# Kernel optimization log

Measured on AMD Instinct MI355X. Metric: run time of the kernel, lower is better.

## Reference

```python
import jax, jax.numpy as jnp
import numpy as np

ALPHA = 0.2          # LeakyReLU negative slope
NEG_INF = -9e15      # mask value used by the torch module


def setup_inputs() -> dict:
    key = jax.random.key(0)
    k_x, k_adj, k_w, k_a = jax.random.split(key, 4)
    B, N, D, L = 8, 2048, 128, 3
    x = jax.random.normal(k_x, (B, N, D), dtype=jnp.float32)
    adj = jax.random.randint(k_adj, (B, N, N), 0, 2, dtype=jnp.int32)
    Wg = jax.random.normal(k_w, (L, D, D), dtype=jnp.float32) * 0.08  # ~Linear init scale
    bg = jnp.zeros((L, D), dtype=jnp.float32)
    attn_a = jax.random.normal(k_a, (L, 2 * D), dtype=jnp.float32) * 0.08
    return {"x": x, "adj": adj, "Wg": Wg, "bg": bg, "attn_a": attn_a}


def reference(x, adj, Wg, bg, attn_a):
    # x: [B,N,D], adj: [B,N,N] int, Wg: [L,D,D], bg: [L,D], attn_a: [L,2D]
    D = x.shape[-1]
    L = Wg.shape[0]
    mask = adj > 0
    for i in range(L):  # small fixed layer loop
        h = jax.nn.relu(x @ Wg[i] + bg[i])                       # [B,N,D]
        # a_input[b,i,j] = [h_i, h_j]; dot with a splits into two rank-1 terms,
        # avoiding the N*N*2D intermediate while computing identical math.
        s1 = h @ attn_a[i, :D]                                   # [B,N]
        s2 = h @ attn_a[i, D:]                                   # [B,N]
        e = jax.nn.leaky_relu(s1[:, :, None] + s2[:, None, :], ALPHA)  # [B,N,N]
        e = jnp.where(mask, e, NEG_INF)
        attn = jax.nn.softmax(e, axis=2)                         # masked softmax over neighbors
        # dropout p=0.0 -> identity
        x = x + jnp.einsum('bij,bjd->bid', attn, h)              # residual update
    return x
```

## Files before the change

kernel.cpp:

```cpp
#include <hip/hip_runtime.h>
#include <stdint.h>

typedef __attribute__((ext_vector_type(8))) short short8;
typedef __attribute__((ext_vector_type(4))) float f32x4;
typedef __attribute__((ext_vector_type(16))) float f32x16;
typedef __attribute__((ext_vector_type(4))) unsigned uint4v;

#define LOG2E 1.4426950408889634f

__device__ __forceinline__ unsigned short f2bf(float f) {
    unsigned u = __float_as_uint(f);
    unsigned r = u + 0x7fffu + ((u >> 16) & 1u);
    return (unsigned short)(r >> 16);
}
__device__ __forceinline__ unsigned fenc(float f) {
    unsigned u = __float_as_uint(f);
    return (u & 0x80000000u) ? ~u : (u | 0x80000000u);
}
__device__ __forceinline__ float fdec(unsigned e) {
    unsigned u = (e & 0x80000000u) ? (e & 0x7fffffffu) : ~e;
    return __uint_as_float(u);
}
__device__ __forceinline__ unsigned cvt_pk_bf16(float lo, float hi) {
    unsigned r;
    asm("v_cvt_pk_bf16_f32 %0, %1, %2" : "=v"(r) : "v"(lo), "v"(hi));
    return r;
}

__global__ __launch_bounds__(256) void k_setup(
    const float* __restrict__ xin, const float* __restrict__ Wf,
    const int* __restrict__ adj, float* __restrict__ xq,
    unsigned short* __restrict__ wTb, unsigned* __restrict__ s2mx,
    unsigned long long* __restrict__ packed)
{
    int blk = blockIdx.x, tid = threadIdx.x;
    if (blk < 2048) {
        int w = (blk * 256 + tid) >> 6;
        int lane = tid & 63;
        for (int k = 0; k < 64; k++) {
            int q = w * 64 + k;
            int row = q >> 5, wd = q & 31;
            int v = adj[row * 2048 + wd * 64 + lane];
            unsigned long long m = __ballot(v > 0);
            if (lane == 0) packed[q] = m;
        }
    } else if (blk < 4096) {
        int e0 = ((blk - 2048) * 256 + tid) * 4;
        *(f32x4*)(xq + e0) = *(const f32x4*)(xin + e0);
    } else if (blk < 4288) {
        int c = (blk - 4096) * 256 + tid;
        int l = c >> 14, rem = c & 16383, n = rem >> 7, k = rem & 127;
        wTb[c] = f2bf(Wf[l * 16384 + k * 128 + n]);
    } else if (tid < 24) {
        s2mx[tid] = fenc(-3e38f);
    }
}

__global__ __launch_bounds__(512) void k_h(
    const float* __restrict__ xq, const unsigned short* __restrict__ wTb,
    const float* __restrict__ bF, const float* __restrict__ aF, int layer,
    unsigned short* __restrict__ hP, float* __restrict__ s1g,
    float* __restrict__ s2g, unsigned* __restrict__ s2mx)
{
    __shared__ short xs[64 * 136];
    __shared__ short wsb[128 * 136];
    __shared__ float s12[2][2][64];
    int blk = blockIdx.x, tid = threadIdx.x;
    int b = blk & 7, rg = blk >> 3;
    int row0 = b * 2048 + rg * 64;
    int lane = tid & 63, quad = lane >> 4, l15 = lane & 15;
    int wv = tid >> 6, rw = wv & 3, ch = wv >> 2;

    for (int c = tid; c < 1024; c += 512) {
        int r = c >> 4, kg = c & 15;
        const float* src = &xq[(row0 + r) * 128 + kg * 8];
        f32x4 v0 = *(const f32x4*)src;
        f32x4 v1 = *(const f32x4*)(src + 4);
        short8 o;
        o[0] = (short)f2bf(v0[0]); o[1] = (short)f2bf(v0[1]);
        o[2] = (short)f2bf(v0[2]); o[3] = (short)f2bf(v0[3]);
        o[4] = (short)f2bf(v1[0]); o[5] = (short)f2bf(v1[1]);
        o[6] = (short)f2bf(v1[2]); o[7] = (short)f2bf(v1[3]);
        *(short8*)&xs[r * 136 + kg * 8] = o;
    }
    const unsigned short* wl = wTb + layer * 16384;
    for (int c = tid; c < 2048; c += 512) {
        int n = c >> 4, kg = c & 15;
        *(short8*)&wsb[n * 136 + kg * 8] = *(const short8*)&wl[n * 128 + kg * 8];
    }
    __syncthreads();

    f32x4 acc[4];
#pragma unroll
    for (int t = 0; t < 4; t++) acc[t] = {0.f, 0.f, 0.f, 0.f};
#pragma unroll
    for (int ks = 0; ks < 4; ks++) {
        short8 af = *(const short8*)&xs[(rw * 16 + l15) * 136 + ks * 32 + quad * 8];
#pragma unroll
        for (int t = 0; t < 4; t++) {
            short8 bf = *(const short8*)&wsb[((ch * 4 + t) * 16 + l15) * 136 + ks * 32 + quad * 8];
            acc[t] = __builtin_amdgcn_mfma_f32_16x16x32_bf16(af, bf, acc[t], 0, 0, 0);
        }
    }

    float s1p[4] = {0.f, 0.f, 0.f, 0.f}, s2p[4] = {0.f, 0.f, 0.f, 0.f};
#pragma unroll
    for (int t = 0; t < 4; t++) {
        int colg = (ch * 4 + t) * 16 + l15;
        float bgf = bF[layer * 128 + colg];
        float a1 = aF[layer * 256 + colg] * LOG2E;
        float a2 = aF[layer * 256 + 128 + colg] * LOG2E;
#pragma unroll
        for (int r = 0; r < 4; r++) {
            float v = acc[t][r] + bgf;
            v = v > 0.f ? v : 0.f;
            acc[t][r] = v;
            s1p[r] = fmaf(v, a1, s1p[r]);
            s2p[r] = fmaf(v, a2, s2p[r]);
        }
    }
#pragma unroll
    for (int r = 0; r < 4; r++) {
#pragma unroll
        for (int off = 1; off < 16; off <<= 1) {
            s1p[r] += __shfl_xor(s1p[r], off, 64);
            s2p[r] += __shfl_xor(s2p[r], off, 64);
        }
    }
    if (l15 == 0) {
#pragma unroll
        for (int r = 0; r < 4; r++) {
            int rloc = rw * 16 + quad * 4 + r;
            s12[0][ch][rloc] = s1p[r];
            s12[1][ch][rloc] = s2p[r];
        }
    }
    __syncthreads();

    short* st = (short*)wsb;
#pragma unroll
    for (int t = 0; t < 4; t++)
#pragma unroll
        for (int r = 0; r < 4; r++)
            st[(rw * 16 + quad * 4 + r) * 130 + (ch * 4 + t) * 16 + l15] = (short)f2bf(acc[t][r]);

    if (tid < 64) {
        float s1 = s12[0][0][tid] + s12[0][1][tid];
        float s2 = s12[1][0][tid] + s12[1][1][tid];
        s1g[row0 + tid] = s1;
        s2g[row0 + tid] = s2;
        float mx = s2;
#pragma unroll
        for (int off = 1; off < 64; off <<= 1)
            mx = fmaxf(mx, __shfl_xor(mx, off, 64));
        if (tid == 0) atomicMax(&s2mx[layer * 8 + b], fenc(mx));
    }
    __syncthreads();
    int jt0 = rg * 4;
    for (int c = tid; c < 1024; c += 512) {
        int t = c >> 8, jl2 = (c >> 6) & 3, sl = c & 63;
        int d = t * 32 + (sl & 31);
        int jloc = jl2 * 16 + (sl >> 5) * 8;
        short8 o;
#pragma unroll
        for (int i = 0; i < 8; i++) o[i] = st[(jloc + i) * 130 + d];
        *(short8*)&hP[(((size_t)(b * 4 + t) * 128 + (jt0 + jl2)) * 64 + sl) * 8] = o;
    }
}

#define GAT_STEP(JL, CUR, NXT)                                                  \
  {                                                                             \
    unsigned b8 = (unsigned)(wdv[CUR] >> joff) & 0xffu;                         \
    float pv[8];                                                                \
    _Pragma("unroll")                                                           \
    for (int jj = 0; jj < 4; jj++) {                                            \
      float v0 = s1fold + sA[CUR][jj];                                          \
      float v1 = s1fold + sB[CUR][jj];                                          \
      pv[jj]     = __builtin_amdgcn_exp2f(fmaxf(v0, fmaf(0.2f, v0, c8)));       \
      pv[jj + 4] = __builtin_amdgcn_exp2f(fmaxf(v1, fmaf(0.2f, v1, c8)));       \
    }                                                                           \
    uint4v pk;                                                                  \
    pk[0] = cvt_pk_bf16(pv[0], pv[1]) & lutq[0][b8];                            \
    pk[1] = cvt_pk_bf16(pv[2], pv[3]) & lutq[1][b8];                            \
    pk[2] = cvt_pk_bf16(pv[4], pv[5]) & lutq[2][b8];                            \
    pk[3] = cvt_pk_bf16(pv[6], pv[7]) & lutq[3][b8];                            \
    short8 af = *(short8*)&pk;                                                  \
    *(short8*)&pshare[CUR][w][lane * 8] = af;                                   \
    ps = __builtin_amdgcn_mfma_f32_32x32x16_bf16(af, onesf, ps, 0, 0, 0);       \
    if ((JL) + 1 < 32) {                                                        \
      wdv[NXT] = prow[(JL) + 1];                                                \
      int j0n = ((JL) + 1) * 64 + joff;                                         \
      sA[NXT] = *(const f32x4*)&s2gb[j0n];                                      \
      sB[NXT] = *(const f32x4*)&s2gb[j0n + 4];                                  \
      _Pragma("unroll")                                                         \
      for (int q = 0; q < 4; q++)                                               \
        bfr[NXT][q] = *(const short8*)&hPb[((size_t)(w * 128 + ((JL) + 1) * 4 + q) * 64 + lane) * 8]; \
    }                                                                           \
    __syncthreads();                                                            \
    _Pragma("unroll")                                                           \
    for (int q = 0; q < 4; q++) {                                               \
      short8 pf = *(short8*)&pshare[CUR][q][lane * 8];                          \
      acc = __builtin_amdgcn_mfma_f32_32x32x16_bf16(pf, bfr[CUR][q], acc, 0, 0, 0); \
    }                                                                           \
  }

__global__ __launch_bounds__(256) void k_attn(
    const unsigned long long* __restrict__ packed,
    const unsigned short* __restrict__ hP, const float* __restrict__ s1g,
    const float* __restrict__ s2g, const unsigned* __restrict__ s2mx,
    int layer, float* __restrict__ xq)
{
    __shared__ unsigned lutq[4][256];
    __shared__ short pshare[2][4][512];
    __shared__ float red_p[4][32];
    int blk = blockIdx.x, tid = threadIdx.x;
    int b = blk & 7, rg = blk >> 3;
    int rowg0 = b * 2048 + rg * 32;
    int w = tid >> 6, lane = tid & 63;
    int col = lane & 31, khalf = lane >> 5;

    {
        unsigned e = (unsigned)tid;
#pragma unroll
        for (int q = 0; q < 4; q++)
            lutq[q][e] = (((e >> (2 * q)) & 1u) ? 0xffffu : 0u) |
                         (((e >> (2 * q + 1)) & 1u) ? 0xffff0000u : 0u);
    }

    float s1v = s1g[rowg0 + col];
    float s2m = fdec(s2mx[layer * 8 + b]);
    float tmh = s1v + s2m;
    float mhat = fmaxf(tmh, 0.2f * tmh);
    float s1fold = s1v - mhat;
    float c8 = -0.8f * mhat;

    short8 onesf;
    {
        short v = (col == 0) ? (short)0x3F80 : (short)0;
        onesf[0]=v;onesf[1]=v;onesf[2]=v;onesf[3]=v;onesf[4]=v;onesf[5]=v;onesf[6]=v;onesf[7]=v;
    }

    const float* s2gb = s2g + b * 2048;
    const unsigned short* hPb = hP + (size_t)b * 4 * 128 * 64 * 8;
    const unsigned long long* prow = packed + (size_t)(rowg0 + col) * 32;
    int joff = w * 16 + khalf * 8;

    f32x16 acc, ps;
#pragma unroll
    for (int r = 0; r < 16; r++) { acc[r] = 0.f; ps[r] = 0.f; }

    unsigned long long wdv[2];
    f32x4 sA[2], sB[2];
    short8 bfr[2][4];

    wdv[0] = prow[0];
    sA[0] = *(const f32x4*)&s2gb[joff];
    sB[0] = *(const f32x4*)&s2gb[joff + 4];
#pragma unroll
    for (int q = 0; q < 4; q++)
        bfr[0][q] = *(const short8*)&hPb[((size_t)(w * 128 + q) * 64 + lane) * 8];
    __syncthreads();

#pragma unroll 1
    for (int jl = 0; jl < 32; jl += 2) {
        GAT_STEP(jl, 0, 1)
        GAT_STEP(jl + 1, 1, 0)
    }

#pragma unroll
    for (int reg = 0; reg < 16; reg++) {
        int row = (reg & 3) + 8 * (reg >> 2) + 4 * khalf;
        if (col == 0) red_p[w][row] = ps[reg];
    }
    __syncthreads();
#pragma unroll
    for (int reg = 0; reg < 16; reg++) {
        int row = (reg & 3) + 8 * (reg >> 2) + 4 * khalf;
        float p = red_p[0][row] + red_p[1][row] + red_p[2][row] + red_p[3][row];
        float rl = p > 0.f ? __builtin_amdgcn_rcpf(p) : 0.f;
        xq[(rowg0 + row) * 128 + w * 32 + col] += acc[reg] * rl;
    }
}

extern "C" void kernel_launch(void* const* d_in, const int* in_sizes, int n_in,
                              void* d_out, int out_size, void* d_ws, size_t ws_size,
                              hipStream_t stream) {
    const void* px = d_in[0];
    int ia = 1; long amax = -1;
    for (int i = 1; i < n_in; i++)
        if ((long)in_sizes[i] > amax) { amax = in_sizes[i]; ia = i; }
    int rem[8]; int m = 0;
    for (int i = 1; i < n_in && m < 8; i++) if (i != ia) rem[m++] = i;
    for (int i = 0; i < m; i++)
        for (int j = i + 1; j < m; j++)
            if (in_sizes[rem[j]] > in_sizes[rem[i]]) { int t = rem[i]; rem[i] = rem[j]; rem[j] = t; }
    const int*   padj = (const int*)((n_in > 1) ? d_in[ia] : d_in[0]);
    const float* pW = (const float*)((m > 0) ? d_in[rem[0]] : d_in[0]);
    const float* pa = (const float*)((m > 1) ? d_in[rem[1]] : d_in[0]);
    const float* pb = (const float*)((m > 2) ? d_in[rem[2]] : d_in[0]);

    float* xq = (float*)d_out;
    char* ws = (char*)d_ws;
    unsigned long long* packed = (unsigned long long*)ws;
    unsigned short* hP = (unsigned short*)(ws + 4194304);
    float* s1 = (float*)(ws + 8388608);
    float* s2 = (float*)(ws + 8454144);
    unsigned* s2mx = (unsigned*)(ws + 8519680);
    unsigned short* wTb = (unsigned short*)(ws + 8519808);

    k_setup<<<4289, 256, 0, stream>>>((const float*)px, pW, padj, xq, wTb, s2mx, packed);
    for (int l = 0; l < 3; l++) {
        k_h<<<256, 512, 0, stream>>>(xq, wTb, pb, pa, l, hP, s1, s2, s2mx);
        k_attn<<<512, 256, 0, stream>>>(packed, hP, s1, s2, s2mx, l, xq);
    }
}
```

Baseline: 315.1 us.

## Split neighbor dimension across waves and reduce partial outputs at end

Before, each wave computed a P tile, shared it through LDS, and after a per-step barrier accumulated one 32-column output slice from all four waves' P tiles. Now each wave handles its own subset of neighbor columns and accumulates all four 32-column output slices locally. A single cross-wave reduction through a 48KB LDS buffer at the end replaces the per-iteration barrier and LDS round trip. This adds accumulator registers (five f32x16) and drops the explicit double-buffered prefetch, relying on unroll 2 and hardware latency hiding, which may lower occupancy.

```diff
diff --git a/kernel.cpp b/kernel.cpp
--- a/kernel.cpp
+++ b/kernel.cpp
@@ -168,42 +168,6 @@
     }
 }
 
-#define GAT_STEP(JL, CUR, NXT)                                                  \
-  {                                                                             \
-    unsigned b8 = (unsigned)(wdv[CUR] >> joff) & 0xffu;                         \
-    float pv[8];                                                                \
-    _Pragma("unroll")                                                           \
-    for (int jj = 0; jj < 4; jj++) {                                            \
-      float v0 = s1fold + sA[CUR][jj];                                          \
-      float v1 = s1fold + sB[CUR][jj];                                          \
-      pv[jj]     = __builtin_amdgcn_exp2f(fmaxf(v0, fmaf(0.2f, v0, c8)));       \
-      pv[jj + 4] = __builtin_amdgcn_exp2f(fmaxf(v1, fmaf(0.2f, v1, c8)));       \
-    }                                                                           \
-    uint4v pk;                                                                  \
-    pk[0] = cvt_pk_bf16(pv[0], pv[1]) & lutq[0][b8];                            \
-    pk[1] = cvt_pk_bf16(pv[2], pv[3]) & lutq[1][b8];                            \
-    pk[2] = cvt_pk_bf16(pv[4], pv[5]) & lutq[2][b8];                            \
-    pk[3] = cvt_pk_bf16(pv[6], pv[7]) & lutq[3][b8];                            \
-    short8 af = *(short8*)&pk;                                                  \
-    *(short8*)&pshare[CUR][w][lane * 8] = af;                                   \
-    ps = __builtin_amdgcn_mfma_f32_32x32x16_bf16(af, onesf, ps, 0, 0, 0);       \
-    if ((JL) + 1 < 32) {                                                        \
-      wdv[NXT] = prow[(JL) + 1];                                                \
-      int j0n = ((JL) + 1) * 64 + joff;                                         \
-      sA[NXT] = *(const f32x4*)&s2gb[j0n];                                      \
-      sB[NXT] = *(const f32x4*)&s2gb[j0n + 4];                                  \
-      _Pragma("unroll")                                                         \
-      for (int q = 0; q < 4; q++)                                               \
-        bfr[NXT][q] = *(const short8*)&hPb[((size_t)(w * 128 + ((JL) + 1) * 4 + q) * 64 + lane) * 8]; \
-    }                                                                           \
-    __syncthreads();                                                            \
-    _Pragma("unroll")                                                           \
-    for (int q = 0; q < 4; q++) {                                               \
-      short8 pf = *(short8*)&pshare[CUR][q][lane * 8];                          \
-      acc = __builtin_amdgcn_mfma_f32_32x32x16_bf16(pf, bfr[CUR][q], acc, 0, 0, 0); \
-    }                                                                           \
-  }
-
 __global__ __launch_bounds__(256) void k_attn(
     const unsigned long long* __restrict__ packed,
     const unsigned short* __restrict__ hP, const float* __restrict__ s1g,
@@ -211,7 +175,7 @@
     int layer, float* __restrict__ xq)
 {
     __shared__ unsigned lutq[4][256];
-    __shared__ short pshare[2][4][512];
+    __shared__ float red[4][3][1024];
     __shared__ float red_p[4][32];
     int blk = blockIdx.x, tid = threadIdx.x;
     int b = blk & 7, rg = blk >> 3;
@@ -245,40 +209,71 @@
     const unsigned long long* prow = packed + (size_t)(rowg0 + col) * 32;
     int joff = w * 16 + khalf * 8;
 
-    f32x16 acc, ps;
-#pragma unroll
-    for (int r = 0; r < 16; r++) { acc[r] = 0.f; ps[r] = 0.f; }
-
-    unsigned long long wdv[2];
-    f32x4 sA[2], sB[2];
-    short8 bfr[2][4];
-
-    wdv[0] = prow[0];
-    sA[0] = *(const f32x4*)&s2gb[joff];
-    sB[0] = *(const f32x4*)&s2gb[joff + 4];
-#pragma unroll
-    for (int q = 0; q < 4; q++)
-        bfr[0][q] = *(const short8*)&hPb[((size_t)(w * 128 + q) * 64 + lane) * 8];
-    __syncthreads();
-
-#pragma unroll 1
-    for (int jl = 0; jl < 32; jl += 2) {
-        GAT_STEP(jl, 0, 1)
-        GAT_STEP(jl + 1, 1, 0)
+    f32x16 z;
+#pragma unroll
+    for (int r = 0; r < 16; r++) z[r] = 0.f;
+    f32x16 acc0 = z, acc1 = z, acc2 = z, acc3 = z, ps = z;
+
+    __syncthreads();
+
+#pragma unroll 2
+    for (int jl = 0; jl < 32; jl++) {
+        int jt = jl * 4 + w;
+        unsigned long long word = prow[jl];
+        unsigned b8 = (unsigned)(word >> joff) & 0xffu;
+        int j0 = jl * 64 + joff;
+        f32x4 sa = *(const f32x4*)&s2gb[j0];
+        f32x4 sb = *(const f32x4*)&s2gb[j0 + 4];
+        const unsigned short* hbase = hPb + ((size_t)jt * 64 + lane) * 8;
+        short8 bf0 = *(const short8*)(hbase);
+        short8 bf1 = *(const short8*)(hbase + 1 * 128 * 64 * 8);
+        short8 bf2 = *(const short8*)(hbase + 2 * 128 * 64 * 8);
+        short8 bf3 = *(const short8*)(hbase + 3 * 128 * 64 * 8);
+        float pv[8];
+#pragma unroll
+        for (int jj = 0; jj < 4; jj++) {
+            float v0 = s1fold + sa[jj];
+            float v1 = s1fold + sb[jj];
+            pv[jj]     = __builtin_amdgcn_exp2f(fmaxf(v0, fmaf(0.2f, v0, c8)));
+            pv[jj + 4] = __builtin_amdgcn_exp2f(fmaxf(v1, fmaf(0.2f, v1, c8)));
+        }
+        uint4v pk;
+        pk[0] = cvt_pk_bf16(pv[0], pv[1]) & lutq[0][b8];
+        pk[1] = cvt_pk_bf16(pv[2], pv[3]) & lutq[1][b8];
+        pk[2] = cvt_pk_bf16(pv[4], pv[5]) & lutq[2][b8];
+        pk[3] = cvt_pk_bf16(pv[6], pv[7]) & lutq[3][b8];
+        short8 af = *(short8*)&pk;
+        ps   = __builtin_amdgcn_mfma_f32_32x32x16_bf16(af, onesf, ps, 0, 0, 0);
+        acc0 = __builtin_amdgcn_mfma_f32_32x32x16_bf16(af, bf0, acc0, 0, 0, 0);
+        acc1 = __builtin_amdgcn_mfma_f32_32x32x16_bf16(af, bf1, acc1, 0, 0, 0);
+        acc2 = __builtin_amdgcn_mfma_f32_32x32x16_bf16(af, bf2, acc2, 0, 0, 0);
+        acc3 = __builtin_amdgcn_mfma_f32_32x32x16_bf16(af, bf3, acc3, 0, 0, 0);
     }
 
 #pragma unroll
     for (int reg = 0; reg < 16; reg++) {
         int row = (reg & 3) + 8 * (reg >> 2) + 4 * khalf;
+        int cidx = row * 32 + col;
         if (col == 0) red_p[w][row] = ps[reg];
+        if (w != 0) red[0][w - 1][cidx] = acc0[reg];
+        if (w != 1) red[1][(w > 1) ? w - 1 : w][cidx] = acc1[reg];
+        if (w != 2) red[2][(w > 2) ? w - 1 : w][cidx] = acc2[reg];
+        if (w != 3) red[3][w][cidx] = acc3[reg];
     }
     __syncthreads();
 #pragma unroll
     for (int reg = 0; reg < 16; reg++) {
         int row = (reg & 3) + 8 * (reg >> 2) + 4 * khalf;
+        int cidx = row * 32 + col;
         float p = red_p[0][row] + red_p[1][row] + red_p[2][row] + red_p[3][row];
         float rl = p > 0.f ? __builtin_amdgcn_rcpf(p) : 0.f;
-        xq[(rowg0 + row) * 128 + w * 32 + col] += acc[reg] * rl;
+        float own;
+        if (w == 0) own = acc0[reg];
+        else if (w == 1) own = acc1[reg];
+        else if (w == 2) own = acc2[reg];
+        else own = acc3[reg];
+        float o = own + red[w][0][cidx] + red[w][1][cidx] + red[w][2][cidx];
+        xq[(rowg0 + row) * 128 + w * 32 + col] += o * rl;
     }
 }
 
```

Measured after the change: 327.9 us. 1.04x slower.

## Stage adjacency bitmask in LDS, use select masking, halve k_h row tile

Applied to the files above, without the earlier changes.

k_attn now copies the block's 32x32 packed adjacency words into shared memory once, instead of each lane fetching a 64-bit mask word from global memory every step. The bf16 LUT-and masking is replaced by per-element selects on the exp results. k_h is retiled to 32 rows per block with 256 threads and twice as many blocks, for more parallelism in the projection kernel. The cost is more repeated W loads across k_h blocks and a few extra VALU selects per step.

```diff
diff --git a/kernel.cpp b/kernel.cpp
--- a/kernel.cpp
+++ b/kernel.cpp
@@ -56,22 +56,22 @@
     }
 }
 
-__global__ __launch_bounds__(512) void k_h(
+__global__ __launch_bounds__(256) void k_h(
     const float* __restrict__ xq, const unsigned short* __restrict__ wTb,
     const float* __restrict__ bF, const float* __restrict__ aF, int layer,
     unsigned short* __restrict__ hP, float* __restrict__ s1g,
     float* __restrict__ s2g, unsigned* __restrict__ s2mx)
 {
-    __shared__ short xs[64 * 136];
+    __shared__ short xs[32 * 136];
     __shared__ short wsb[128 * 136];
-    __shared__ float s12[2][2][64];
+    __shared__ float s12[2][2][32];
     int blk = blockIdx.x, tid = threadIdx.x;
     int b = blk & 7, rg = blk >> 3;
-    int row0 = b * 2048 + rg * 64;
+    int row0 = b * 2048 + rg * 32;
     int lane = tid & 63, quad = lane >> 4, l15 = lane & 15;
-    int wv = tid >> 6, rw = wv & 3, ch = wv >> 2;
-
-    for (int c = tid; c < 1024; c += 512) {
+    int wv = tid >> 6, rw = wv & 1, ch = wv >> 1;
+
+    for (int c = tid; c < 512; c += 256) {
         int r = c >> 4, kg = c & 15;
         const float* src = &xq[(row0 + r) * 128 + kg * 8];
         f32x4 v0 = *(const f32x4*)src;
@@ -84,7 +84,7 @@
         *(short8*)&xs[r * 136 + kg * 8] = o;
     }
     const unsigned short* wl = wTb + layer * 16384;
-    for (int c = tid; c < 2048; c += 512) {
+    for (int c = tid; c < 2048; c += 256) {
         int n = c >> 4, kg = c & 15;
         *(short8*)&wsb[n * 136 + kg * 8] = *(const short8*)&wl[n * 128 + kg * 8];
     }
@@ -144,21 +144,21 @@
         for (int r = 0; r < 4; r++)
             st[(rw * 16 + quad * 4 + r) * 130 + (ch * 4 + t) * 16 + l15] = (short)f2bf(acc[t][r]);
 
-    if (tid < 64) {
+    if (tid < 32) {
         float s1 = s12[0][0][tid] + s12[0][1][tid];
         float s2 = s12[1][0][tid] + s12[1][1][tid];
         s1g[row0 + tid] = s1;
         s2g[row0 + tid] = s2;
         float mx = s2;
 #pragma unroll
-        for (int off = 1; off < 64; off <<= 1)
+        for (int off = 1; off < 32; off <<= 1)
             mx = fmaxf(mx, __shfl_xor(mx, off, 64));
         if (tid == 0) atomicMax(&s2mx[layer * 8 + b], fenc(mx));
     }
     __syncthreads();
-    int jt0 = rg * 4;
-    for (int c = tid; c < 1024; c += 512) {
-        int t = c >> 8, jl2 = (c >> 6) & 3, sl = c & 63;
+    int jt0 = rg * 2;
+    for (int c = tid; c < 512; c += 256) {
+        int t = c >> 7, jl2 = (c >> 6) & 1, sl = c & 63;
         int d = t * 32 + (sl & 31);
         int jloc = jl2 * 16 + (sl >> 5) * 8;
         short8 o;
@@ -170,25 +170,27 @@
 
 #define GAT_STEP(JL, CUR, NXT)                                                  \
   {                                                                             \
-    unsigned b8 = (unsigned)(wdv[CUR] >> joff) & 0xffu;                         \
+    unsigned long long word = pmask[col][JL];                                   \
+    unsigned b8 = (unsigned)(word >> joff) & 0xffu;                             \
     float pv[8];                                                                \
     _Pragma("unroll")                                                           \
     for (int jj = 0; jj < 4; jj++) {                                            \
       float v0 = s1fold + sA[CUR][jj];                                          \
       float v1 = s1fold + sB[CUR][jj];                                          \
-      pv[jj]     = __builtin_amdgcn_exp2f(fmaxf(v0, fmaf(0.2f, v0, c8)));       \
-      pv[jj + 4] = __builtin_amdgcn_exp2f(fmaxf(v1, fmaf(0.2f, v1, c8)));       \
+      float e0 = __builtin_amdgcn_exp2f(fmaxf(v0, fmaf(0.2f, v0, c8)));         \
+      float e1 = __builtin_amdgcn_exp2f(fmaxf(v1, fmaf(0.2f, v1, c8)));         \
+      pv[jj]     = ((b8 >> jj) & 1u) ? e0 : 0.f;                                \
+      pv[jj + 4] = ((b8 >> (jj + 4)) & 1u) ? e1 : 0.f;                          \
     }                                                                           \
     uint4v pk;                                                                  \
-    pk[0] = cvt_pk_bf16(pv[0], pv[1]) & lutq[0][b8];                            \
-    pk[1] = cvt_pk_bf16(pv[2], pv[3]) & lutq[1][b8];                            \
-    pk[2] = cvt_pk_bf16(pv[4], pv[5]) & lutq[2][b8];                            \
-    pk[3] = cvt_pk_bf16(pv[6], pv[7]) & lutq[3][b8];                            \
+    pk[0] = cvt_pk_bf16(pv[0], pv[1]);                                          \
+    pk[1] = cvt_pk_bf16(pv[2], pv[3]);                                          \
+    pk[2] = cvt_pk_bf16(pv[4], pv[5]);                                          \
+    pk[3] = cvt_pk_bf16(pv[6], pv[7]);                                          \
     short8 af = *(short8*)&pk;                                                  \
     *(short8*)&pshare[CUR][w][lane * 8] = af;                                   \
     ps = __builtin_amdgcn_mfma_f32_32x32x16_bf16(af, onesf, ps, 0, 0, 0);       \
     if ((JL) + 1 < 32) {                                                        \
-      wdv[NXT] = prow[(JL) + 1];                                                \
       int j0n = ((JL) + 1) * 64 + joff;                                         \
       sA[NXT] = *(const f32x4*)&s2gb[j0n];                                      \
       sB[NXT] = *(const f32x4*)&s2gb[j0n + 4];                                  \
@@ -210,8 +212,8 @@
     const float* __restrict__ s2g, const unsigned* __restrict__ s2mx,
     int layer, float* __restrict__ xq)
 {
-    __shared__ unsigned lutq[4][256];
     __shared__ short pshare[2][4][512];
+    __shared__ unsigned long long pmask[32][33];
     __shared__ float red_p[4][32];
     int blk = blockIdx.x, tid = threadIdx.x;
     int b = blk & 7, rg = blk >> 3;
@@ -219,12 +221,9 @@
     int w = tid >> 6, lane = tid & 63;
     int col = lane & 31, khalf = lane >> 5;
 
-    {
-        unsigned e = (unsigned)tid;
-#pragma unroll
-        for (int q = 0; q < 4; q++)
-            lutq[q][e] = (((e >> (2 * q)) & 1u) ? 0xffffu : 0u) |
-                         (((e >> (2 * q + 1)) & 1u) ? 0xffff0000u : 0u);
+    for (int c = tid; c < 1024; c += 256) {
+        int r = c >> 5, wd = c & 31;
+        pmask[r][wd] = packed[(size_t)(rowg0 + r) * 32 + wd];
     }
 
     float s1v = s1g[rowg0 + col];
@@ -242,18 +241,15 @@
 
     const float* s2gb = s2g + b * 2048;
     const unsigned short* hPb = hP + (size_t)b * 4 * 128 * 64 * 8;
-    const unsigned long long* prow = packed + (size_t)(rowg0 + col) * 32;
     int joff = w * 16 + khalf * 8;
 
     f32x16 acc, ps;
 #pragma unroll
     for (int r = 0; r < 16; r++) { acc[r] = 0.f; ps[r] = 0.f; }
 
-    unsigned long long wdv[2];
     f32x4 sA[2], sB[2];
     short8 bfr[2][4];
 
-    wdv[0] = prow[0];
     sA[0] = *(const f32x4*)&s2gb[joff];
     sB[0] = *(const f32x4*)&s2gb[joff + 4];
 #pragma unroll
@@ -310,7 +306,7 @@
 
     k_setup<<<4289, 256, 0, stream>>>((const float*)px, pW, padj, xq, wTb, s2mx, packed);
     for (int l = 0; l < 3; l++) {
-        k_h<<<256, 512, 0, stream>>>(xq, wTb, pb, pa, l, hP, s1, s2, s2mx);
+        k_h<<<512, 256, 0, stream>>>(xq, wTb, pb, pa, l, hP, s1, s2, s2mx);
         k_attn<<<512, 256, 0, stream>>>(packed, hP, s1, s2, s2mx, l, xq);
     }
 }
```

Result: no change. 319.5 us (+1.4%).
